# Kernel optimization log

Measured on AMD Instinct MI355X. Metric: run time of the kernel, lower is better.

## Reference

```python
import jax, jax.numpy as jnp
import numpy as np

D = 128
N_ATOMS = 200000
E_ATOMS = 800000
G = 2000            # num molecule graphs = nDrug + nProtein
N_BIG = 7000        # nDrug + nProtein + nSe
E_BIG = 200000
N_EMB = 100001


def _edges(key, n, e):
    # random edges guaranteed to have no self-loops (PyG convs strip/re-add them)
    k1, k2 = jax.random.split(key)
    src = jax.random.randint(k1, (e,), 0, n)
    off = jax.random.randint(k2, (e,), 1, n)
    return jnp.stack([src, (src + off) % n])


def setup_inputs() -> dict:
    key = jax.random.key(0)
    ks = jax.random.split(key, 40)
    s = 0.09  # ~1/sqrt(D) init scale
    nrm = lambda i, shape: jax.random.normal(ks[i], shape, dtype=jnp.float32) * s
    inp = {}
    inp['x_ids'] = jax.random.randint(ks[0], (N_BIG,), 0, N_EMB)
    inp['drugEdges'] = _edges(ks[1], N_BIG, E_BIG)
    inp['seEdges'] = _edges(ks[2], 5000, 1000)  # unused by forward
    inp['drugNodes'] = jax.random.randint(ks[3], (1000,), 0, N_BIG)
    inp['seNodes'] = jax.random.randint(ks[4], (5000,), 0, N_BIG)
    inp['proteinNodes'] = jax.random.randint(ks[5], (1000,), 0, N_EMB)
    inp['proteinWeight'] = jax.random.normal(ks[6], (1000,), dtype=jnp.float32)
    inp['atom_x'] = jax.random.randint(ks[7], (N_ATOMS,), 0, N_EMB)
    inp['atom_edge_index'] = _edges(ks[8], N_ATOMS, E_ATOMS)
    inp['atom_batch'] = jnp.sort(jax.random.randint(ks[9], (N_ATOMS,), 0, G))
    inp['nDrug'] = 1000
    inp['emb'] = jax.random.uniform(ks[10], (N_EMB, D), minval=0.001, maxval=0.3, dtype=jnp.float32)
    for i in range(3):
        inp[f'gatW{i+1}'] = nrm(11 + i, (D, D))
        inp[f'attS{i+1}'] = nrm(14 + i, (D,))
        inp[f'attD{i+1}'] = nrm(17 + i, (D,))
        inp[f'gatB{i+1}'] = nrm(20 + i, (D,))
        inp[f'poolP{i+1}'] = nrm(23 + i, (D,))
    inp['lin1_W'] = nrm(26, (2 * D, D))
    inp['lin1_b'] = nrm(27, (D,))
    inp['gcn1_W'] = nrm(28, (D, D))
    inp['gcn1_b'] = nrm(29, (D,))
    inp['gcn2_W'] = nrm(30, (D, D))
    inp['gcn2_b'] = nrm(31, (D,))
    return inp


def _gat(x, src, dst, n, W, a_s, a_d, b):
    # PyG GATConv, 1 head: h = xW; e_ij = LeakyReLU(a_s.h_j + a_d.h_i);
    # softmax over incoming edges of i (self-loops re-added); out_i = sum_j alpha_ij h_j + b
    h = x @ W
    loops = jnp.arange(n)
    s = jnp.concatenate([src, loops])
    d = jnp.concatenate([dst, loops])
    e = jax.nn.leaky_relu((h @ a_s)[s] + (h @ a_d)[d], 0.2)
    m = jax.ops.segment_max(e, d, num_segments=n)
    ex = jnp.exp(e - m[d])
    z = jax.ops.segment_sum(ex, d, num_segments=n)
    w = ex / z[d]
    return jax.ops.segment_sum(w[:, None] * h[s], d, num_segments=n) + b


def _gcn(x, src, dst, n, W, b):
    loops = jnp.arange(n)
    s = jnp.concatenate([src, loops])
    d = jnp.concatenate([dst, loops])
    deg = jax.ops.segment_sum(jnp.ones(d.shape[0], x.dtype), d, num_segments=n)
    dis = deg ** -0.5
    coef = dis[s] * dis[d]
    return jax.ops.segment_sum(coef[:, None] * (x @ W)[s], d, num_segments=n) + b


def _topk1(x, p):
    # TopKPooling with ratio=1: keep all nodes, gate by tanh of projection score
    score = (x @ p) / jnp.linalg.norm(p)
    return x * jnp.tanh(score)[:, None]


def _gmp_gap(x, batch, g):
    mx = jax.ops.segment_max(x, batch, num_segments=g)
    sm = jax.ops.segment_sum(x, batch, num_segments=g)
    cnt = jax.ops.segment_sum(jnp.ones((x.shape[0], 1), x.dtype), batch, num_segments=g)
    return jnp.concatenate([mx, sm / jnp.maximum(cnt, 1.0)], axis=1)


def reference(x_ids, drugEdges, seEdges, drugNodes, seNodes, proteinNodes, proteinWeight,
              atom_x, atom_edge_index, atom_batch, nDrug, emb,
              gatW1, attS1, attD1, gatB1, poolP1,
              gatW2, attS2, attD2, gatB2, poolP2,
              gatW3, attS3, attD3, gatB3, poolP3,
              lin1_W, lin1_b, gcn1_W, gcn1_b, gcn2_W, gcn2_b):
    na = atom_x.shape[0]
    asrc, adst = atom_edge_index[0], atom_edge_index[1]
    xa = emb[atom_x]                                   # [na, D]
    xa = jax.nn.relu(_gat(xa, asrc, adst, na, gatW1, attS1, attD1, gatB1))
    xa = _topk1(xa, poolP1)
    x1 = _gmp_gap(xa, atom_batch, G)                   # [G, 2D]
    xa = jax.nn.relu(_gat(xa, asrc, adst, na, gatW2, attS2, attD2, gatB2))
    xa = _topk1(xa, poolP2)
    x2 = _gmp_gap(xa, atom_batch, G)
    xa = jax.nn.relu(_gat(xa, asrc, adst, na, gatW3, attS3, attD3, gatB3))
    xa = _topk1(xa, poolP3)
    x3 = _gmp_gap(xa, atom_batch, G)
    xDP = jax.nn.relu((x1 + x2 + x3) @ lin1_W + lin1_b)  # [G, D]
    nProtein = proteinNodes.shape[0]
    xse = emb[x_ids[nDrug + nProtein:]]                # side-effect node embeddings
    xb = jnp.concatenate([xDP, xse], axis=0)           # [N_BIG, D]
    dsrc, ddst = drugEdges[0], drugEdges[1]
    xb = jax.nn.relu(_gcn(xb, dsrc, ddst, N_BIG, gcn1_W, gcn1_b))
    xb = jax.nn.relu(_gcn(xb, dsrc, ddst, N_BIG, gcn2_W, gcn2_b))
    return (xb[drugNodes], xb[seNodes], xb)
```

## Files before the change

kernel.cpp:

```cpp
#include <hip/hip_runtime.h>
#include <cfloat>
#include <cmath>

#define D 128
#define N_ATOMS 200000
#define E_ATOMS 800000
#define G_GROUPS 2000
#define N_BIG 7000
#define E_BIG 200000
#define N_ALL (N_ATOMS + N_BIG)
#define E_ALL (E_ATOMS + E_BIG)

static inline int ceil_div(int a, int b) { return (a + b - 1) / b; }

typedef __attribute__((ext_vector_type(8))) _Float16 f16x8;
typedef __attribute__((ext_vector_type(2))) _Float16 h2_t;
typedef __attribute__((ext_vector_type(4))) float f32x4;

__device__ inline h2_t u2h(unsigned u) { return __builtin_bit_cast(h2_t, u); }
__device__ inline unsigned h2u(h2_t h) { return __builtin_bit_cast(unsigned, h); }
__device__ inline unsigned packh2(float x, float y) {
  h2_t h;
  h[0] = (_Float16)x;
  h[1] = (_Float16)y;
  return h2u(h);
}
__device__ inline float leaky(float e) { return fmaxf(e, 0.2f * e); }
__device__ inline float fast_tanh(float x) {
  float cx = fminf(fmaxf(x, -15.f), 15.f);
  float t = __expf(2.f * cx);
  return (t - 1.f) * __frcp_rn(t + 1.f);
}

__global__ void count_all(const int* __restrict__ adst, const int* __restrict__ ddst, int* __restrict__ deg,
                          int* __restrict__ rank) {
  int i = blockIdx.x * 256 + threadIdx.x;
  if (i < E_ATOMS)
    rank[i] = atomicAdd(&deg[adst[i]], 1);
  else if (i < E_ALL)
    rank[i] = atomicAdd(&deg[N_ATOMS + ddst[i - E_ATOMS]], 1);
}

__global__ void fill_csx(const int* __restrict__ asrc, const int* __restrict__ adst,
                         const int* __restrict__ dsrc, const int* __restrict__ ddst,
                         const int* __restrict__ rpx, const int* __restrict__ rank, int* __restrict__ csx) {
  int i = blockIdx.x * 256 + threadIdx.x;
  if (i < E_ATOMS) {
    csx[rpx[adst[i]] + rank[i]] = asrc[i];
  } else if (i < E_ALL) {
    int k = i - E_ATOMS;
    csx[rpx[N_ATOMS + ddst[k]] + rank[i]] = dsrc[k];
  }
}

__global__ void fill_pad(const int* __restrict__ deg, const int* __restrict__ rpx, int* __restrict__ csx) {
  int d = blockIdx.x * 256 + threadIdx.x;
  if (d >= N_ALL) return;
  int dg = deg[d];
  int b = rpx[d], e = rpx[d + 1];
  int sv = (d < N_ATOMS) ? d : d - N_ATOMS;
  for (int j = b + dg; j < e; ++j) csx[j] = sv;
}

__global__ void post_count(const int* __restrict__ deg, int* __restrict__ cntp, float* __restrict__ dis) {
  int i = blockIdx.x * 256 + threadIdx.x;
  if (i < N_ALL) cntp[i] = (deg[i] + 8) & ~7;
  if (i < N_BIG) dis[i] = 1.f / sqrtf((float)(deg[N_ATOMS + i] + 1));
}

__global__ __launch_bounds__(256) void scan_phase1(const int* __restrict__ in, int* __restrict__ out,
                                                   int* __restrict__ bsums, int n) {
  __shared__ int lds[256];
  int t = threadIdx.x;
  int base = blockIdx.x * 1024;
  int v[4];
  int s = 0;
#pragma unroll
  for (int j = 0; j < 4; ++j) {
    int i = base + t * 4 + j;
    v[j] = (i < n) ? in[i] : 0;
    s += v[j];
  }
  lds[t] = s;
  __syncthreads();
  for (int off = 1; off < 256; off <<= 1) {
    int x = (t >= off) ? lds[t - off] : 0;
    __syncthreads();
    lds[t] += x;
    __syncthreads();
  }
  int excl = lds[t] - s;
  if (t == 255) bsums[blockIdx.x] = lds[255];
  int run = excl;
#pragma unroll
  for (int j = 0; j < 4; ++j) {
    int i = base + t * 4 + j;
    if (i < n) out[i] = run;
    run += v[j];
  }
}

__global__ __launch_bounds__(256) void scan_phase2(int* __restrict__ bsums, int* __restrict__ total_out, int nb) {
  __shared__ int lds[256];
  int t = threadIdx.x;
  int s = (t < nb) ? bsums[t] : 0;
  lds[t] = s;
  __syncthreads();
  for (int off = 1; off < 256; off <<= 1) {
    int x = (t >= off) ? lds[t - off] : 0;
    __syncthreads();
    lds[t] += x;
    __syncthreads();
  }
  if (t < nb) bsums[t] = lds[t] - s;
  if (t == 255) total_out[0] = lds[255];
}

__global__ void scan_phase3(int* __restrict__ out, const int* __restrict__ bsums, int n) {
  int i = blockIdx.x * 256 + threadIdx.x;
  if (i < n) out[i] += bsums[i >> 10];
}

__global__ __launch_bounds__(256) void prep_kernel(const float* __restrict__ W0, const float* __restrict__ W1,
                                                   const float* __restrict__ W2, const float* __restrict__ W3,
                                                   const float* __restrict__ W4, unsigned short* __restrict__ Wsplit,
                                                   const float* __restrict__ p0, const float* __restrict__ p1,
                                                   const float* __restrict__ p2, float* __restrict__ pn) {
  int b = blockIdx.x;
  if (b < 5) {
    const float* W = (b == 0) ? W0 : (b == 1) ? W1 : (b == 2) ? W2 : (b == 3) ? W3 : W4;
    unsigned short* dstH = Wsplit + (size_t)b * 16384;
    int t = threadIdx.x;
    int col = t & 127;
    int half = t >> 7;
#pragma unroll
    for (int kg = 0; kg < 8; ++kg) {
      int k0 = kg * 16 + half * 8;
      f16x8 vh;
#pragma unroll
      for (int j = 0; j < 8; ++j) vh[j] = (_Float16)W[(k0 + j) * 128 + col];
      int byte_off = (col * 256 + k0 * 2) ^ ((col & 7) << 4);
      *(f16x8*)((char*)dstH + byte_off) = vh;
    }
  } else {
    int t = threadIdx.x;
    int g = t >> 6, lane = t & 63;
    if (g < 3) {
      const float* p = (g == 0) ? p0 : (g == 1) ? p1 : p2;
      float2 v = ((const float2*)p)[lane];
      float s = v.x * v.x + v.y * v.y;
#pragma unroll
      for (int off = 32; off; off >>= 1) s += __shfl_xor(s, off);
      if (lane == 0) pn[g] = 1.f / sqrtf(s);
    }
  }
}

__global__ __launch_bounds__(512) void gemm_f16(const unsigned short* __restrict__ A,
                                                const unsigned short* __restrict__ Wsp,
                                                unsigned short* __restrict__ H, float* __restrict__ hs,
                                                float* __restrict__ hd, const float* __restrict__ aS,
                                                const float* __restrict__ aD, int M) {
  __shared__ unsigned short Wl[16384];
  int t = threadIdx.x;
  {
    const uint4* src = (const uint4*)Wsp;
    uint4* dst = (uint4*)Wl;
#pragma unroll
    for (int i = 0; i < 4; ++i) dst[t + i * 512] = src[t + i * 512];
  }
  __syncthreads();
  int wave = t >> 6, lane = t & 63;
  int lr = lane & 15, lq = lane >> 4;
  int row0 = blockIdx.x * 256 + wave * 32;
  f32x4 acc[2][8];
#pragma unroll
  for (int rt = 0; rt < 2; ++rt)
#pragma unroll
    for (int ct = 0; ct < 8; ++ct) acc[rt][ct] = (f32x4){0.f, 0.f, 0.f, 0.f};

#pragma unroll
  for (int ks = 0; ks < 4; ++ks) {
    int k8 = ks * 32 + lq * 8;
    f16x8 Af[2];
#pragma unroll
    for (int rt = 0; rt < 2; ++rt) {
      int row = row0 + rt * 16 + lr;
      if (row < M) {
        Af[rt] = *(const f16x8*)(A + (size_t)row * D + k8);
      } else {
        Af[rt] = (f16x8){0, 0, 0, 0, 0, 0, 0, 0};
      }
    }
#pragma unroll
    for (int ct = 0; ct < 8; ++ct) {
      int col = ct * 16 + lr;
      int byte_off = (col * 256 + k8 * 2) ^ ((col & 7) << 4);
      f16x8 Bh = *(f16x8*)((char*)Wl + byte_off);
#pragma unroll
      for (int rt = 0; rt < 2; ++rt)
        acc[rt][ct] = __builtin_amdgcn_mfma_f32_16x16x32_f16(Af[rt], Bh, acc[rt][ct], 0, 0, 0);
    }
  }
#pragma unroll
  for (int rt = 0; rt < 2; ++rt)
#pragma unroll
    for (int ct = 0; ct < 8; ++ct) {
      int col = ct * 16 + lr;
#pragma unroll
      for (int i = 0; i < 4; ++i) {
        int row = row0 + rt * 16 + lq * 4 + i;
        if (row < M) {
          _Float16 hv = (_Float16)acc[rt][ct][i];
          H[(size_t)row * D + col] = __builtin_bit_cast(unsigned short, hv);
        }
      }
    }
  if (aS) {
    float sA[8], sD[8];
#pragma unroll
    for (int ct = 0; ct < 8; ++ct) {
      sA[ct] = aS[ct * 16 + lr];
      sD[ct] = aD[ct * 16 + lr];
    }
#pragma unroll
    for (int rt = 0; rt < 2; ++rt)
#pragma unroll
      for (int i = 0; i < 4; ++i) {
        float ps = 0.f, pd = 0.f;
#pragma unroll
        for (int ct = 0; ct < 8; ++ct) {
          ps = fmaf(acc[rt][ct][i], sA[ct], ps);
          pd = fmaf(acc[rt][ct][i], sD[ct], pd);
        }
#pragma unroll
        for (int off = 1; off < 16; off <<= 1) {
          ps += __shfl_xor(ps, off);
          pd += __shfl_xor(pd, off);
        }
        int row = row0 + rt * 16 + lq * 4 + i;
        if (lr == 0 && row < M) {
          hs[row] = ps;
          hd[row] = pd;
        }
      }
  }
}

__global__ void gcn_weights(const int* __restrict__ rpx, const int* __restrict__ deg,
                            const int* __restrict__ csx, const float* __restrict__ dis,
                            unsigned* __restrict__ wtsG, int N) {
  int dl = blockIdx.x * 256 + threadIdx.x;
  if (dl >= N) return;
  int d = N_ATOMS + dl;
  int b = rpx[d];
  int cnt = rpx[d + 1] - b;
  int dg = deg[d];
  float dd = dis[dl];
  for (int j = 0; j < dg; ++j) {
    float w = dis[csx[b + j]] * dd;
    wtsG[b + j] = packh2(w, w);
  }
  wtsG[b + dg] = packh2(dd * dd, dd * dd);
  for (int j = dg + 1; j < cnt; ++j) wtsG[b + j] = 0;
}

__global__ __launch_bounds__(256) void gat_fused(const unsigned short* __restrict__ H,
                                                 const int* __restrict__ rpx, const int* __restrict__ deg,
                                                 const int* __restrict__ csx, const float* __restrict__ hs,
                                                 const float* __restrict__ hd, const float* __restrict__ bias,
                                                 const float* __restrict__ poolP, const float* __restrict__ pnL,
                                                 unsigned short* __restrict__ Xout, int N) {
  int wid = (blockIdx.x * 256 + threadIdx.x) >> 6;
  int d = __builtin_amdgcn_readfirstlane(wid);
  if (d >= N) return;
  int lane = threadIdx.x & 63;
  int rb = rpx[d];
  int cnt = rpx[d + 1] - rb;
  int dg = deg[d];
  float hdd = hd[d];
  const unsigned* H2 = (const unsigned*)H;
  float ax = 0.f, ay = 0.f;
  float iz;
  if (cnt <= 64) {
    float e = -FLT_MAX;
    if (lane < dg)
      e = leaky(hs[csx[rb + lane]] + hdd);
    else if (lane == dg)
      e = leaky(hs[d] + hdd);
    float m = e;
#pragma unroll
    for (int off = 32; off; off >>= 1) m = fmaxf(m, __shfl_xor(m, off));
    float w = (lane <= dg) ? __expf(e - m) : 0.f;
    float z = w;
#pragma unroll
    for (int off = 32; off; off >>= 1) z += __shfl_xor(z, off);
    iz = 1.f / z;
    unsigned wpk = packh2(w, w);
    for (int i = 0; i < cnt; i += 8) {
      int s0 = csx[rb + i + 0], s1 = csx[rb + i + 1], s2 = csx[rb + i + 2], s3 = csx[rb + i + 3];
      int s4 = csx[rb + i + 4], s5 = csx[rb + i + 5], s6 = csx[rb + i + 6], s7 = csx[rb + i + 7];
      unsigned w0 = __shfl(wpk, i + 0), w1 = __shfl(wpk, i + 1), w2 = __shfl(wpk, i + 2),
               w3 = __shfl(wpk, i + 3), w4 = __shfl(wpk, i + 4), w5 = __shfl(wpk, i + 5),
               w6 = __shfl(wpk, i + 6), w7 = __shfl(wpk, i + 7);
      unsigned h0 = H2[(size_t)s0 * 64 + lane];
      unsigned h1 = H2[(size_t)s1 * 64 + lane];
      unsigned h2 = H2[(size_t)s2 * 64 + lane];
      unsigned h3 = H2[(size_t)s3 * 64 + lane];
      unsigned h4 = H2[(size_t)s4 * 64 + lane];
      unsigned h5 = H2[(size_t)s5 * 64 + lane];
      unsigned h6 = H2[(size_t)s6 * 64 + lane];
      unsigned h7 = H2[(size_t)s7 * 64 + lane];
      h2_t a2 = u2h(w0) * u2h(h0);
      a2 += u2h(w1) * u2h(h1);
      a2 += u2h(w2) * u2h(h2);
      a2 += u2h(w3) * u2h(h3);
      h2_t b2h = u2h(w4) * u2h(h4);
      b2h += u2h(w5) * u2h(h5);
      b2h += u2h(w6) * u2h(h6);
      b2h += u2h(w7) * u2h(h7);
      a2 += b2h;
      ax += (float)a2[0];
      ay += (float)a2[1];
    }
  } else {
    float ml = -FLT_MAX;
    for (int j = lane; j < dg; j += 64) ml = fmaxf(ml, leaky(hs[csx[rb + j]] + hdd));
    if (lane == 0) ml = fmaxf(ml, leaky(hs[d] + hdd));
#pragma unroll
    for (int off = 32; off; off >>= 1) ml = fmaxf(ml, __shfl_xor(ml, off));
    float zl = 0.f;
    for (int j = lane; j < dg; j += 64) zl += __expf(leaky(hs[csx[rb + j]] + hdd) - ml);
    if (lane == 0) zl += __expf(leaky(hs[d] + hdd) - ml);
#pragma unroll
    for (int off = 32; off; off >>= 1) zl += __shfl_xor(zl, off);
    iz = 1.f / zl;
    for (int i = 0; i <= dg; ++i) {
      int s = csx[rb + i];
      float ev = (i < dg) ? leaky(hs[s] + hdd) : leaky(hs[d] + hdd);
      float wv = __expf(ev - ml);
      h2_t hv = u2h(H2[(size_t)s * 64 + lane]);
      ax = fmaf(wv, (float)hv[0], ax);
      ay = fmaf(wv, (float)hv[1], ay);
    }
  }
  float2 b2 = ((const float2*)bias)[lane];
  ax = fmaxf(fmaf(ax, iz, b2.x), 0.f);
  ay = fmaxf(fmaf(ay, iz, b2.y), 0.f);
  float2 p2 = ((const float2*)poolP)[lane];
  float dot = ax * p2.x + ay * p2.y;
#pragma unroll
  for (int off = 32; off; off >>= 1) dot += __shfl_xor(dot, off);
  float sc = fast_tanh(dot * pnL[0]);
  ((unsigned*)Xout)[(size_t)d * 64 + lane] = packh2(ax * sc, ay * sc);
}

__global__ __launch_bounds__(256) void gcn_gather(const unsigned short* __restrict__ Y,
                                                  const int* __restrict__ rpx, const int* __restrict__ csx,
                                                  const unsigned* __restrict__ wtsG, const float* __restrict__ b,
                                                  unsigned short* __restrict__ outB, float* __restrict__ outF,
                                                  int N) {
  int wid = (blockIdx.x * 256 + threadIdx.x) >> 6;
  int dl = __builtin_amdgcn_readfirstlane(wid);
  if (dl >= N) return;
  int lane = threadIdx.x & 63;
  int rb = rpx[N_ATOMS + dl];
  int cnt = rpx[N_ATOMS + dl + 1] - rb;
  const unsigned* Y2 = (const unsigned*)Y;
  float ax = 0.f, ay = 0.f;
  for (int i = 0; i < cnt; i += 8) {
    int s0 = csx[rb + i + 0], s1 = csx[rb + i + 1], s2 = csx[rb + i + 2], s3 = csx[rb + i + 3];
    int s4 = csx[rb + i + 4], s5 = csx[rb + i + 5], s6 = csx[rb + i + 6], s7 = csx[rb + i + 7];
    unsigned w0 = wtsG[rb + i + 0], w1 = wtsG[rb + i + 1], w2 = wtsG[rb + i + 2], w3 = wtsG[rb + i + 3];
    unsigned w4 = wtsG[rb + i + 4], w5 = wtsG[rb + i + 5], w6 = wtsG[rb + i + 6], w7 = wtsG[rb + i + 7];
    unsigned h0 = Y2[(size_t)s0 * 64 + lane];
    unsigned h1 = Y2[(size_t)s1 * 64 + lane];
    unsigned h2 = Y2[(size_t)s2 * 64 + lane];
    unsigned h3 = Y2[(size_t)s3 * 64 + lane];
    unsigned h4 = Y2[(size_t)s4 * 64 + lane];
    unsigned h5 = Y2[(size_t)s5 * 64 + lane];
    unsigned h6 = Y2[(size_t)s6 * 64 + lane];
    unsigned h7 = Y2[(size_t)s7 * 64 + lane];
    h2_t a2 = u2h(w0) * u2h(h0);
    a2 += u2h(w1) * u2h(h1);
    a2 += u2h(w2) * u2h(h2);
    a2 += u2h(w3) * u2h(h3);
    h2_t b2h = u2h(w4) * u2h(h4);
    b2h += u2h(w5) * u2h(h5);
    b2h += u2h(w6) * u2h(h6);
    b2h += u2h(w7) * u2h(h7);
    a2 += b2h;
    ax += (float)a2[0];
    ay += (float)a2[1];
  }
  float2 b2 = ((const float2*)b)[lane];
  float ox = fmaxf(ax + b2.x, 0.f);
  float oy = fmaxf(ay + b2.y, 0.f);
  if (outF)
    ((float2*)outF)[(size_t)dl * 64 + lane] = make_float2(ox, oy);
  else
    ((unsigned*)outB)[(size_t)dl * 64 + lane] = packh2(ox, oy);
}

__global__ void group_bounds(const int* __restrict__ batch, int* __restrict__ gs, int* __restrict__ ge, int n) {
  int i = blockIdx.x * 256 + threadIdx.x;
  if (i >= n) return;
  int b = batch[i];
  if (i == 0 || batch[i - 1] != b) gs[b] = i;
  if (i == n - 1 || batch[i + 1] != b) ge[b] = i + 1;
}

__global__ __launch_bounds__(256) void pool_kernel(const unsigned short* __restrict__ X,
                                                   const int* __restrict__ gs, const int* __restrict__ ge,
                                                   float* __restrict__ x123) {
  __shared__ float2 mxs[4][64];
  __shared__ float2 sms[4][64];
  int g = blockIdx.x;
  int wv = threadIdx.x >> 6;
  int p = threadIdx.x & 63;
  int beg = gs[g], end = ge[g];
  int cnt = end - beg;
  const unsigned* X2 = (const unsigned*)X;
  float mx0 = -FLT_MAX, mx1 = -FLT_MAX, sm0 = 0.f, sm1 = 0.f;
  for (int i = beg + wv; i < end; i += 4) {
    h2_t v = u2h(X2[(size_t)i * 64 + p]);
    float a = (float)v[0], b = (float)v[1];
    mx0 = fmaxf(mx0, a);
    mx1 = fmaxf(mx1, b);
    sm0 += a;
    sm1 += b;
  }
  mxs[wv][p] = make_float2(mx0, mx1);
  sms[wv][p] = make_float2(sm0, sm1);
  __syncthreads();
  if (threadIdx.x < 64 && cnt > 0) {
#pragma unroll
    for (int k = 1; k < 4; ++k) {
      float2 m2 = mxs[k][p], s2 = sms[k][p];
      mx0 = fmaxf(mx0, m2.x);
      mx1 = fmaxf(mx1, m2.y);
      sm0 += s2.x;
      sm1 += s2.y;
    }
    float inv = 1.f / (float)cnt;
    float* xg = x123 + (size_t)g * 256;
    xg[2 * p] += mx0;
    xg[2 * p + 1] += mx1;
    xg[128 + 2 * p] += sm0 * inv;
    xg[128 + 2 * p + 1] += sm1 * inv;
  }
}

__global__ __launch_bounds__(128) void lin1_kernel(const float* __restrict__ x123, const float* __restrict__ W,
                                                   const float* __restrict__ b, unsigned short* __restrict__ xb) {
  __shared__ float row[256];
  int g = blockIdx.x;
  int c = threadIdx.x;
  row[c] = x123[(size_t)g * 256 + c];
  row[c + 128] = x123[(size_t)g * 256 + 128 + c];
  __syncthreads();
  float acc = b[c];
#pragma unroll 8
  for (int k = 0; k < 256; ++k) acc = fmaf(row[k], W[k * 128 + c], acc);
  _Float16 hv = (_Float16)fmaxf(acc, 0.f);
  xb[(size_t)g * D + c] = __builtin_bit_cast(unsigned short, hv);
}

__global__ void xse_kernel(const float* __restrict__ emb, const int* __restrict__ x_ids,
                           const int* __restrict__ nDrugPtr, int nProtein, unsigned short* __restrict__ xb) {
  int idx = blockIdx.x * 256 + threadIdx.x;
  int r = idx >> 6, lane = idx & 63;
  int off = nDrugPtr[0] + nProtein;
  int id = x_ids[off + r];
  float2 v = ((const float2*)(emb + (size_t)id * D))[lane];
  ((unsigned*)xb)[(size_t)(G_GROUPS + r) * 64 + lane] = packh2(v.x, v.y);
}

__global__ void gather_emb(const float* __restrict__ emb, const int* __restrict__ ids,
                           unsigned short* __restrict__ out, int n) {
  int idx = blockIdx.x * 256 + threadIdx.x;
  int node = idx >> 5, lane = idx & 31;
  if (node >= n) return;
  float4 v = ((const float4*)(emb + (size_t)ids[node] * D))[lane];
  uint2 o;
  o.x = packh2(v.x, v.y);
  o.y = packh2(v.z, v.w);
  ((uint2*)out)[(size_t)node * 32 + lane] = o;
}

__global__ void out_gather(const float* __restrict__ xb, const int* __restrict__ dn, const int* __restrict__ sn,
                           float* __restrict__ out) {
  int idx = blockIdx.x * 256 + threadIdx.x;
  int r = idx >> 6, lane = idx & 63;
  int s = (r < 1000) ? dn[r] : (r < 6000) ? sn[r - 1000] : (r - 6000);
  ((float2*)out)[(size_t)idx] = ((const float2*)(xb + (size_t)s * D))[lane];
}

extern "C" void kernel_launch(void* const* d_in, const int* in_sizes, int n_in, void* d_out, int out_size,
                              void* d_ws, size_t ws_size, hipStream_t stream) {
  const int* x_ids = (const int*)d_in[0];
  const int* drugE = (const int*)d_in[1];
  const int* drugNodes = (const int*)d_in[3];
  const int* seNodes = (const int*)d_in[4];
  int nProtein = in_sizes[5];
  const int* atom_x = (const int*)d_in[7];
  const int* atomE = (const int*)d_in[8];
  const int* atom_batch = (const int*)d_in[9];
  const int* nDrugPtr = (const int*)d_in[10];
  const float* emb = (const float*)d_in[11];
  const float* gatW[3] = {(const float*)d_in[12], (const float*)d_in[17], (const float*)d_in[22]};
  const float* attS[3] = {(const float*)d_in[13], (const float*)d_in[18], (const float*)d_in[23]};
  const float* attD[3] = {(const float*)d_in[14], (const float*)d_in[19], (const float*)d_in[24]};
  const float* gatB[3] = {(const float*)d_in[15], (const float*)d_in[20], (const float*)d_in[25]};
  const float* poolP[3] = {(const float*)d_in[16], (const float*)d_in[21], (const float*)d_in[26]};
  const float* lin1_W = (const float*)d_in[27];
  const float* lin1_b = (const float*)d_in[28];
  const float* gcn1_W = (const float*)d_in[29];
  const float* gcn1_b = (const float*)d_in[30];
  const float* gcn2_W = (const float*)d_in[31];
  const float* gcn2_b = (const float*)d_in[32];
  float* out = (float*)d_out;
  (void)n_in; (void)out_size; (void)ws_size;

  const int MAXX = E_ALL + 8 * N_ALL;

  char* ws = (char*)d_ws;
  size_t off = 0;
  auto alloc = [&](size_t bytes) -> char* {
    char* p = ws + off;
    off += (bytes + 255) & ~(size_t)255;
    return p;
  };
  unsigned short* bufA = (unsigned short*)alloc((size_t)N_ATOMS * D * 2);
  unsigned short* bufB = (unsigned short*)alloc((size_t)N_ATOMS * D * 2);
  float* hs = (float*)alloc((size_t)N_ATOMS * 4);
  float* hd = (float*)alloc((size_t)N_ATOMS * 4);
  int* csx = (int*)alloc((size_t)MAXX * 4);
  unsigned* wtsG = (unsigned*)alloc((size_t)MAXX * 4);
  int* rank = (int*)alloc((size_t)E_ALL * 4);
  float* x123 = (float*)alloc((size_t)G_GROUPS * 256 * 4);
  unsigned short* xb1 = (unsigned short*)alloc((size_t)N_BIG * D * 2);
  unsigned short* xb2 = (unsigned short*)alloc((size_t)N_BIG * D * 2);
  float* xbF = (float*)alloc((size_t)N_BIG * D * 4);
  unsigned short* Wsplit = (unsigned short*)alloc((size_t)5 * 16384 * 2);
  int* rpx = (int*)alloc((size_t)(N_ALL + 1) * 4);
  int* deg = (int*)alloc((size_t)N_ALL * 4);
  int* cntp = (int*)alloc((size_t)N_ALL * 4);
  float* disB = (float*)alloc((size_t)N_BIG * 4);
  int* gs = (int*)alloc((size_t)G_GROUPS * 4);
  int* ge = (int*)alloc((size_t)G_GROUPS * 4);
  int* bsums = (int*)alloc(256 * 4);
  float* pn = (float*)alloc(256);

  const int* asrc = atomE;
  const int* adst = atomE + E_ATOMS;
  const int* dsrc = drugE;
  const int* ddst = drugE + E_BIG;

  prep_kernel<<<6, 256, 0, stream>>>(gatW[0], gatW[1], gatW[2], gcn1_W, gcn2_W, Wsplit, poolP[0], poolP[1],
                                     poolP[2], pn);

  hipMemsetAsync(deg, 0, (size_t)N_ALL * 4, stream);
  count_all<<<ceil_div(E_ALL, 256), 256, 0, stream>>>(adst, ddst, deg, rank);
  post_count<<<ceil_div(N_ALL, 256), 256, 0, stream>>>(deg, cntp, disB);
  scan_phase1<<<ceil_div(N_ALL, 1024), 256, 0, stream>>>(cntp, rpx, bsums, N_ALL);
  scan_phase2<<<1, 256, 0, stream>>>(bsums, rpx + N_ALL, ceil_div(N_ALL, 1024));
  scan_phase3<<<ceil_div(N_ALL, 256), 256, 0, stream>>>(rpx, bsums, N_ALL);
  fill_csx<<<ceil_div(E_ALL, 256), 256, 0, stream>>>(asrc, adst, dsrc, ddst, rpx, rank, csx);
  fill_pad<<<ceil_div(N_ALL, 256), 256, 0, stream>>>(deg, rpx, csx);
  gcn_weights<<<ceil_div(N_BIG, 256), 256, 0, stream>>>(rpx, deg, csx, disB, wtsG, N_BIG);

  hipMemsetAsync(gs, 0, (size_t)G_GROUPS * 4, stream);
  hipMemsetAsync(ge, 0, (size_t)G_GROUPS * 4, stream);
  group_bounds<<<ceil_div(N_ATOMS, 256), 256, 0, stream>>>(atom_batch, gs, ge, N_ATOMS);

  gather_emb<<<ceil_div(N_ATOMS * 32, 256), 256, 0, stream>>>(emb, atom_x, bufA, N_ATOMS);
  hipMemsetAsync(x123, 0, (size_t)G_GROUPS * 256 * 4, stream);

  for (int L = 0; L < 3; ++L) {
    gemm_f16<<<ceil_div(N_ATOMS, 256), 512, 0, stream>>>(bufA, Wsplit + (size_t)L * 16384, bufB, hs, hd,
                                                         attS[L], attD[L], N_ATOMS);
    gat_fused<<<N_ATOMS * 64 / 256, 256, 0, stream>>>(bufB, rpx, deg, csx, hs, hd, gatB[L], poolP[L], pn + L,
                                                      bufA, N_ATOMS);
    pool_kernel<<<G_GROUPS, 256, 0, stream>>>(bufA, gs, ge, x123);
  }

  lin1_kernel<<<G_GROUPS, 128, 0, stream>>>(x123, lin1_W, lin1_b, xb1);
  xse_kernel<<<(N_BIG - G_GROUPS) * 64 / 256, 256, 0, stream>>>(emb, x_ids, nDrugPtr, nProtein, xb1);

  gemm_f16<<<ceil_div(N_BIG, 256), 512, 0, stream>>>(xb1, Wsplit + (size_t)3 * 16384, bufB, nullptr, nullptr,
                                                     nullptr, nullptr, N_BIG);
  gcn_gather<<<N_BIG * 64 / 256, 256, 0, stream>>>(bufB, rpx, csx, wtsG, gcn1_b, xb2, nullptr, N_BIG);
  gemm_f16<<<ceil_div(N_BIG, 256), 512, 0, stream>>>(xb2, Wsplit + (size_t)4 * 16384, bufB, nullptr, nullptr,
                                                     nullptr, nullptr, N_BIG);
  gcn_gather<<<N_BIG * 64 / 256, 256, 0, stream>>>(bufB, rpx, csx, wtsG, gcn2_b, nullptr, xbF, N_BIG);

  out_gather<<<13000 * 64 / 256, 256, 0, stream>>>(xbF, drugNodes, seNodes, out);
}
```

Before: 541.6 us.

## Compute GAT edge softmax weights block-cooperatively in LDS without max subtraction

The GAT aggregation kernel now has each 256-thread block handle four destination nodes. The block first computes the exponentiated attention weights for all of their edges in parallel into shared memory, and each wave then reads weights from LDS instead of doing per-wave shuffles and reductions. The softmax max-subtraction is dropped, which relies on the logits being small enough not to overflow. Weights are stored in half precision, and the normaliser is summed serially per wave. Index arithmetic is also switched from size_t to 32-bit ints in both gather kernels to cut address computation.

```diff
diff --git a/kernel.cpp b/kernel.cpp
--- a/kernel.cpp
+++ b/kernel.cpp
@@ -10,6 +10,7 @@
 #define E_BIG 200000
 #define N_ALL (N_ATOMS + N_BIG)
 #define E_ALL (E_ATOMS + E_BIG)
+#define MAXE 2048
 
 static inline int ceil_div(int a, int b) { return (a + b - 1) / b; }
 
@@ -271,46 +272,64 @@
                                                  const float* __restrict__ hd, const float* __restrict__ bias,
                                                  const float* __restrict__ poolP, const float* __restrict__ pnL,
                                                  unsigned short* __restrict__ Xout, int N) {
-  int wid = (blockIdx.x * 256 + threadIdx.x) >> 6;
-  int d = __builtin_amdgcn_readfirstlane(wid);
+  __shared__ int l_rp[5];
+  __shared__ int l_dg[4];
+  __shared__ float l_hd[4];
+  __shared__ unsigned l_w[MAXE];
+  int tid = threadIdx.x;
+  int d0 = blockIdx.x * 4;
+  if (tid < 5) l_rp[tid] = rpx[min(d0 + tid, N)];
+  if (tid >= 8 && tid < 12) {
+    int k = tid - 8;
+    int dk = d0 + k;
+    l_dg[k] = (dk < N) ? deg[dk] : 0;
+    l_hd[k] = (dk < N) ? hd[dk] : 0.f;
+  }
+  __syncthreads();
+  int base = l_rp[0];
+  int total = l_rp[4] - base;
+  bool fallback = (total > MAXE);
+  if (!fallback) {
+    for (int j = tid; j < total; j += 256) {
+      int off = base + j;
+      int k = (off >= l_rp[2]) ? 2 : 0;
+      if (off >= l_rp[k + 1]) k += 1;
+      int local = off - l_rp[k];
+      int dg = l_dg[k];
+      float w = 0.f;
+      if (local < dg)
+        w = __expf(leaky(hs[csx[off]] + l_hd[k]));
+      else if (local == dg)
+        w = __expf(leaky(hs[d0 + k] + l_hd[k]));
+      l_w[j] = packh2(w, w);
+    }
+  }
+  __syncthreads();
+  int wv = __builtin_amdgcn_readfirstlane(tid >> 6);
+  int lane = tid & 63;
+  int d = d0 + wv;
   if (d >= N) return;
-  int lane = threadIdx.x & 63;
-  int rb = rpx[d];
-  int cnt = rpx[d + 1] - rb;
-  int dg = deg[d];
-  float hdd = hd[d];
+  int rb = __builtin_amdgcn_readfirstlane(l_rp[wv]);
+  int cnt = __builtin_amdgcn_readfirstlane(l_rp[wv + 1]) - rb;
+  int lb = rb - base;
   const unsigned* H2 = (const unsigned*)H;
   float ax = 0.f, ay = 0.f;
-  float iz;
-  if (cnt <= 64) {
-    float e = -FLT_MAX;
-    if (lane < dg)
-      e = leaky(hs[csx[rb + lane]] + hdd);
-    else if (lane == dg)
-      e = leaky(hs[d] + hdd);
-    float m = e;
-#pragma unroll
-    for (int off = 32; off; off >>= 1) m = fmaxf(m, __shfl_xor(m, off));
-    float w = (lane <= dg) ? __expf(e - m) : 0.f;
-    float z = w;
-#pragma unroll
-    for (int off = 32; off; off >>= 1) z += __shfl_xor(z, off);
-    iz = 1.f / z;
-    unsigned wpk = packh2(w, w);
+  float z = 0.f;
+  if (!fallback) {
+    for (int i = 0; i < cnt; ++i) z += (float)u2h(l_w[lb + i])[0];
     for (int i = 0; i < cnt; i += 8) {
       int s0 = csx[rb + i + 0], s1 = csx[rb + i + 1], s2 = csx[rb + i + 2], s3 = csx[rb + i + 3];
       int s4 = csx[rb + i + 4], s5 = csx[rb + i + 5], s6 = csx[rb + i + 6], s7 = csx[rb + i + 7];
-      unsigned w0 = __shfl(wpk, i + 0), w1 = __shfl(wpk, i + 1), w2 = __shfl(wpk, i + 2),
-               w3 = __shfl(wpk, i + 3), w4 = __shfl(wpk, i + 4), w5 = __shfl(wpk, i + 5),
-               w6 = __shfl(wpk, i + 6), w7 = __shfl(wpk, i + 7);
-      unsigned h0 = H2[(size_t)s0 * 64 + lane];
-      unsigned h1 = H2[(size_t)s1 * 64 + lane];
-      unsigned h2 = H2[(size_t)s2 * 64 + lane];
-      unsigned h3 = H2[(size_t)s3 * 64 + lane];
-      unsigned h4 = H2[(size_t)s4 * 64 + lane];
-      unsigned h5 = H2[(size_t)s5 * 64 + lane];
-      unsigned h6 = H2[(size_t)s6 * 64 + lane];
-      unsigned h7 = H2[(size_t)s7 * 64 + lane];
+      unsigned w0 = l_w[lb + i + 0], w1 = l_w[lb + i + 1], w2 = l_w[lb + i + 2], w3 = l_w[lb + i + 3];
+      unsigned w4 = l_w[lb + i + 4], w5 = l_w[lb + i + 5], w6 = l_w[lb + i + 6], w7 = l_w[lb + i + 7];
+      unsigned h0 = H2[s0 * 64 + lane];
+      unsigned h1 = H2[s1 * 64 + lane];
+      unsigned h2 = H2[s2 * 64 + lane];
+      unsigned h3 = H2[s3 * 64 + lane];
+      unsigned h4 = H2[s4 * 64 + lane];
+      unsigned h5 = H2[s5 * 64 + lane];
+      unsigned h6 = H2[s6 * 64 + lane];
+      unsigned h7 = H2[s7 * 64 + lane];
       h2_t a2 = u2h(w0) * u2h(h0);
       a2 += u2h(w1) * u2h(h1);
       a2 += u2h(w2) * u2h(h2);
@@ -324,26 +343,19 @@
       ay += (float)a2[1];
     }
   } else {
-    float ml = -FLT_MAX;
-    for (int j = lane; j < dg; j += 64) ml = fmaxf(ml, leaky(hs[csx[rb + j]] + hdd));
-    if (lane == 0) ml = fmaxf(ml, leaky(hs[d] + hdd));
-#pragma unroll
-    for (int off = 32; off; off >>= 1) ml = fmaxf(ml, __shfl_xor(ml, off));
-    float zl = 0.f;
-    for (int j = lane; j < dg; j += 64) zl += __expf(leaky(hs[csx[rb + j]] + hdd) - ml);
-    if (lane == 0) zl += __expf(leaky(hs[d] + hdd) - ml);
-#pragma unroll
-    for (int off = 32; off; off >>= 1) zl += __shfl_xor(zl, off);
-    iz = 1.f / zl;
+    int dg = l_dg[wv];
+    float hdd = l_hd[wv];
     for (int i = 0; i <= dg; ++i) {
       int s = csx[rb + i];
       float ev = (i < dg) ? leaky(hs[s] + hdd) : leaky(hs[d] + hdd);
-      float wv = __expf(ev - ml);
-      h2_t hv = u2h(H2[(size_t)s * 64 + lane]);
-      ax = fmaf(wv, (float)hv[0], ax);
-      ay = fmaf(wv, (float)hv[1], ay);
-    }
-  }
+      float wv2 = __expf(ev);
+      z += wv2;
+      h2_t hv = u2h(H2[s * 64 + lane]);
+      ax = fmaf(wv2, (float)hv[0], ax);
+      ay = fmaf(wv2, (float)hv[1], ay);
+    }
+  }
+  float iz = 1.f / z;
   float2 b2 = ((const float2*)bias)[lane];
   ax = fmaxf(fmaf(ax, iz, b2.x), 0.f);
   ay = fmaxf(fmaf(ay, iz, b2.y), 0.f);
@@ -352,7 +364,7 @@
 #pragma unroll
   for (int off = 32; off; off >>= 1) dot += __shfl_xor(dot, off);
   float sc = fast_tanh(dot * pnL[0]);
-  ((unsigned*)Xout)[(size_t)d * 64 + lane] = packh2(ax * sc, ay * sc);
+  ((unsigned*)Xout)[d * 64 + lane] = packh2(ax * sc, ay * sc);
 }
 
 __global__ __launch_bounds__(256) void gcn_gather(const unsigned short* __restrict__ Y,
@@ -373,14 +385,14 @@
     int s4 = csx[rb + i + 4], s5 = csx[rb + i + 5], s6 = csx[rb + i + 6], s7 = csx[rb + i + 7];
     unsigned w0 = wtsG[rb + i + 0], w1 = wtsG[rb + i + 1], w2 = wtsG[rb + i + 2], w3 = wtsG[rb + i + 3];
     unsigned w4 = wtsG[rb + i + 4], w5 = wtsG[rb + i + 5], w6 = wtsG[rb + i + 6], w7 = wtsG[rb + i + 7];
-    unsigned h0 = Y2[(size_t)s0 * 64 + lane];
-    unsigned h1 = Y2[(size_t)s1 * 64 + lane];
-    unsigned h2 = Y2[(size_t)s2 * 64 + lane];
-    unsigned h3 = Y2[(size_t)s3 * 64 + lane];
-    unsigned h4 = Y2[(size_t)s4 * 64 + lane];
-    unsigned h5 = Y2[(size_t)s5 * 64 + lane];
-    unsigned h6 = Y2[(size_t)s6 * 64 + lane];
-    unsigned h7 = Y2[(size_t)s7 * 64 + lane];
+    unsigned h0 = Y2[s0 * 64 + lane];
+    unsigned h1 = Y2[s1 * 64 + lane];
+    unsigned h2 = Y2[s2 * 64 + lane];
+    unsigned h3 = Y2[s3 * 64 + lane];
+    unsigned h4 = Y2[s4 * 64 + lane];
+    unsigned h5 = Y2[s5 * 64 + lane];
+    unsigned h6 = Y2[s6 * 64 + lane];
+    unsigned h7 = Y2[s7 * 64 + lane];
     h2_t a2 = u2h(w0) * u2h(h0);
     a2 += u2h(w1) * u2h(h1);
     a2 += u2h(w2) * u2h(h2);
@@ -580,8 +592,8 @@
   for (int L = 0; L < 3; ++L) {
     gemm_f16<<<ceil_div(N_ATOMS, 256), 512, 0, stream>>>(bufA, Wsplit + (size_t)L * 16384, bufB, hs, hd,
                                                          attS[L], attD[L], N_ATOMS);
-    gat_fused<<<N_ATOMS * 64 / 256, 256, 0, stream>>>(bufB, rpx, deg, csx, hs, hd, gatB[L], poolP[L], pn + L,
-                                                      bufA, N_ATOMS);
+    gat_fused<<<ceil_div(N_ATOMS, 4), 256, 0, stream>>>(bufB, rpx, deg, csx, hs, hd, gatB[L], poolP[L],
+                                                        pn + L, bufA, N_ATOMS);
     pool_kernel<<<G_GROUPS, 256, 0, stream>>>(bufA, gs, ge, x123);
   }
 
```

New measurement: 565.6 us. 4.4% more time.
